# Kernel optimization log

Hardware: AMD Instinct MI355X
Metric: run time of the kernel (lower is better)

## Reference

```python
import jax, jax.numpy as jnp
import numpy as np

N = 200000   # active voxels
K = 27       # 3^3 kernel offsets
C = 64       # feature channels (in == out -> residual is Identity)
EPS = 1e-5   # BatchNorm eps (torch default)


def setup_inputs() -> dict:
    key = jax.random.key(0)
    k0, k1, k2, k3 = jax.random.split(key, 4)
    x = jax.random.normal(k0, (N, C), dtype=jnp.float32)
    # neighbor map: for each output voxel and kernel offset, index of input voxel
    nbr_idx = jax.random.randint(k1, (N, K), 0, N, dtype=jnp.int64)
    W1 = jax.random.normal(k2, (K, C, C), dtype=jnp.float32) * 0.05
    W2 = jax.random.normal(k3, (K, C, C), dtype=jnp.float32) * 0.05
    gamma1 = jnp.ones((C,), jnp.float32)
    beta1 = jnp.zeros((C,), jnp.float32)
    gamma2 = jnp.ones((C,), jnp.float32)
    beta2 = jnp.zeros((C,), jnp.float32)
    return {"x": x, "nbr_idx": nbr_idx, "W1": W1, "gamma1": gamma1,
            "beta1": beta1, "W2": W2, "gamma2": gamma2, "beta2": beta2}


def batchnorm(x, gamma, beta):
    # train-mode BatchNorm1d over the voxel axis (biased variance)
    mu = x.mean(axis=0)
    var = x.var(axis=0)
    return (x - mu) * jax.lax.rsqrt(var + EPS) * gamma + beta


def sparse_conv(x, nbr_idx, W):
    # gather-GEMM-scatter sparse conv, streamed over the 27 kernel offsets
    # x: [N, Cin], nbr_idx: [N, K], W: [K, Cin, Cout]
    def body(acc, kw):
        idx, Wk = kw                      # idx: [N], Wk: [Cin, Cout]
        return acc + x[idx] @ Wk, None
    acc0 = jnp.zeros((x.shape[0], W.shape[2]), x.dtype)
    acc, _ = jax.lax.scan(body, acc0, (nbr_idx.T, W))
    return acc


def reference(x, nbr_idx, W1, gamma1, beta1, W2, gamma2, beta2):
    residual = x  # in_features == out_features -> Identity residual
    out = sparse_conv(jax.nn.relu(batchnorm(x, gamma1, beta1)), nbr_idx, W1)
    out = sparse_conv(jax.nn.relu(batchnorm(out, gamma2, beta2)), nbr_idx, W2)
    return out + residual
```

## Files before the change

kernel.cpp:

```cpp
#include <hip/hip_runtime.h>


#define KOFF 27

typedef __bf16 bf16x8 __attribute__((ext_vector_type(8)));
typedef float floatx4 __attribute__((ext_vector_type(4)));

__device__ __forceinline__ unsigned short f2bf(float x) {
    union { float f; unsigned int u; } v; v.f = x;
    unsigned int u = v.u;
    unsigned int r = u + 0x7FFFu + ((u >> 16) & 1u);
    return (unsigned short)(r >> 16);
}
__device__ __forceinline__ float bf2f(unsigned short s) {
    union { float f; unsigned int u; } v; v.u = ((unsigned int)s) << 16; return v.f;
}

__global__ void prep2(const float* __restrict__ W1, const float* __restrict__ W2,
                      unsigned short* __restrict__ W1f, unsigned short* __restrict__ W2f,
                      const float* __restrict__ x, float* __restrict__ stats,
                      int total) {
    int b = blockIdx.x, t = threadIdx.x;
    if (b < 54) {
        __shared__ float sW[64 * 68];
        int k = b % 27;
        const float* src = (b < 27 ? W1 : W2) + k * 4096;
        unsigned short* dst = (b < 27 ? W1f : W2f) + (size_t)k * 4096;
        #pragma unroll
        for (int i = 0; i < 4; ++i) {
            int i4 = t + i * 256;
            float4 v = ((const float4*)src)[i4];
            int f = i4 * 4, r = f >> 6, c = f & 63;
            sW[r * 68 + c]     = v.x;
            sW[r * 68 + c + 1] = v.y;
            sW[r * 68 + c + 2] = v.z;
            sW[r * 68 + c + 3] = v.w;
        }
        __syncthreads();
        int fi = (t >> 5) & 7, ct = fi >> 1, ks = fi & 1;
        unsigned short o[16];
        #pragma unroll
        for (int d = 0; d < 2; ++d) {
            int lane2 = (t * 2 + d) & 63, q = lane2 >> 4, l15 = lane2 & 15;
            #pragma unroll
            for (int j = 0; j < 8; ++j) {
                int cin = ks * 32 + q * 8 + j, cout = ct * 16 + l15;
                o[d * 8 + j] = f2bf(sW[cin * 68 + cout]);
            }
        }
        ((uint4*)(dst + t * 16))[0] = *(const uint4*)(o);
        ((uint4*)(dst + t * 16))[1] = *(const uint4*)(o + 8);
        return;
    }
    __shared__ float s[128];
    if (t < 128) s[t] = 0.f;
    __syncthreads();
    int i = (b - 54) * 256 + t;
    int stride = (gridDim.x - 54) * 256;
    int c = i & 63;
    float s1 = 0.f, s2 = 0.f;
    for (; i < total; i += stride) { float v = x[i]; s1 += v; s2 += v * v; }
    atomicAdd(&s[c], s1);
    atomicAdd(&s[64 + c], s2);
    __syncthreads();
    if (t < 64) { atomicAdd(&stats[t], s[t]); atomicAdd(&stats[64 + t], s[64 + t]); }
}

__global__ void bn_relu_f32(const float* __restrict__ in, const float* __restrict__ sums,
                            const float* __restrict__ gamma, const float* __restrict__ beta,
                            unsigned short* __restrict__ out, int total4, float invN) {
    __shared__ float sab[128];
    int t = threadIdx.x;
    if (t < 64) {
        float mu  = sums[t] * invN;
        float var = fmaxf(sums[64 + t] * invN - mu * mu, 0.f);
        float a   = gamma[t] * rsqrtf(var + 1e-5f);
        sab[t] = a; sab[64 + t] = beta[t] - mu * a;
    }
    __syncthreads();
    int i = blockIdx.x * blockDim.x + t;
    int stride = gridDim.x * blockDim.x;
    for (; i < total4; i += stride) {
        float4 v = ((const float4*)in)[i];
        int c0 = (i << 2) & 63;
        ushort4 o;
        o.x = f2bf(fmaxf(sab[c0]     * v.x + sab[64 + c0],     0.f));
        o.y = f2bf(fmaxf(sab[c0 + 1] * v.y + sab[64 + c0 + 1], 0.f));
        o.z = f2bf(fmaxf(sab[c0 + 2] * v.z + sab[64 + c0 + 2], 0.f));
        o.w = f2bf(fmaxf(sab[c0 + 3] * v.w + sab[64 + c0 + 3], 0.f));
        ((ushort4*)out)[i] = o;
    }
}

__global__ void bn_relu_b16(const unsigned short* __restrict__ in, const float* __restrict__ sums,
                            const float* __restrict__ gamma, const float* __restrict__ beta,
                            unsigned short* __restrict__ out, int total8, float invN) {
    __shared__ float sab[128];
    int t = threadIdx.x;
    if (t < 64) {
        float mu  = sums[t] * invN;
        float var = fmaxf(sums[64 + t] * invN - mu * mu, 0.f);
        float a   = gamma[t] * rsqrtf(var + 1e-5f);
        sab[t] = a; sab[64 + t] = beta[t] - mu * a;
    }
    __syncthreads();
    int i = blockIdx.x * blockDim.x + t;
    int stride = gridDim.x * blockDim.x;
    for (; i < total8; i += stride) {
        uint4 v = ((const uint4*)in)[i];
        int c0 = (i << 3) & 63;
        unsigned int w[4] = {v.x, v.y, v.z, v.w};
        unsigned int o[4];
        #pragma unroll
        for (int p = 0; p < 4; ++p) {
            float f0 = bf2f((unsigned short)(w[p] & 0xffff));
            float f1 = bf2f((unsigned short)(w[p] >> 16));
            int c = c0 + p * 2;
            unsigned short r0 = f2bf(fmaxf(sab[c]     * f0 + sab[64 + c],     0.f));
            unsigned short r1 = f2bf(fmaxf(sab[c + 1] * f1 + sab[64 + c + 1], 0.f));
            o[p] = (unsigned int)r0 | ((unsigned int)r1 << 16);
        }
        ((uint4*)out)[i] = make_uint4(o[0], o[1], o[2], o[3]);
    }
}

#define MFMA(a, b, c) __builtin_amdgcn_mfma_f32_16x16x32_bf16(a, b, c, 0, 0, 0)
#define WAIT_LGKM0() __builtin_amdgcn_s_waitcnt(0xC07F)

__global__ __launch_bounds__(256, 4) void spconv(
        const unsigned short* __restrict__ h,
        const int* __restrict__ idx,
        const unsigned short* __restrict__ Wf,
        unsigned short* __restrict__ outb,
        float* __restrict__ outf,
        const float* __restrict__ resid,
        float* __restrict__ stats,
        int N) {
    __shared__ unsigned short sB[2][4096];
    __shared__ float sE[128 * 68];
    __shared__ float sred[128];
    int t = threadIdx.x, lane = t & 63, wid = t >> 6;
    int q = lane >> 4, l15 = lane & 15;
    int base = blockIdx.x * 128;
    if (t < 128) sred[t] = 0.f;

    int r0 = base + wid * 32 + l15;
    int r1 = r0 + 16;
    const int* ip0 = idx + (size_t)min(r0, N - 1) * KOFF;
    const int* ip1 = idx + (size_t)min(r1, N - 1) * KOFF;
    int qo = q * 8;

    floatx4 acc[2][4];
    #pragma unroll
    for (int a_ = 0; a_ < 2; ++a_)
        #pragma unroll
        for (int b_ = 0; b_ < 4; ++b_)
            acc[a_][b_] = floatx4{0.f, 0.f, 0.f, 0.f};

    bf16x8 A0[4], A1[4], A2[4];
    {
        int g0 = ip0[0], g1 = ip1[0];
        const unsigned short* p0 = h + ((size_t)g0 << 6) + qo;
        const unsigned short* p1 = h + ((size_t)g1 << 6) + qo;
        A0[0] = *(const bf16x8*)p0; A0[1] = *(const bf16x8*)(p0 + 32);
        A0[2] = *(const bf16x8*)p1; A0[3] = *(const bf16x8*)(p1 + 32);
        g0 = ip0[1]; g1 = ip1[1];
        p0 = h + ((size_t)g0 << 6) + qo;
        p1 = h + ((size_t)g1 << 6) + qo;
        A1[0] = *(const bf16x8*)p0; A1[1] = *(const bf16x8*)(p0 + 32);
        A1[2] = *(const bf16x8*)p1; A1[3] = *(const bf16x8*)(p1 + 32);
    }
    int gc0 = ip0[2], gc1 = ip1[2];

    const uint4* Wf4 = (const uint4*)Wf;
    int bo = wid * 128 + lane * 2;
    uint4 bs0 = Wf4[bo], bs1 = Wf4[bo + 1];
    ((uint4*)sB[0])[bo] = bs0; ((uint4*)sB[0])[bo + 1] = bs1;
    bs0 = Wf4[512 + bo]; bs1 = Wf4[512 + bo + 1];

#define COMPUTE(ACUR, CB) {                                                    \
    const bf16x8* bp = (const bf16x8*)sB[CB];                                  \
    bf16x8 f0 = bp[lane], f1 = bp[64 + lane], f2 = bp[128 + lane], f3 = bp[192 + lane]; \
    acc[0][0] = MFMA(ACUR[0], f0, acc[0][0]); acc[0][0] = MFMA(ACUR[1], f1, acc[0][0]); \
    acc[0][1] = MFMA(ACUR[0], f2, acc[0][1]); acc[0][1] = MFMA(ACUR[1], f3, acc[0][1]); \
    acc[1][0] = MFMA(ACUR[2], f0, acc[1][0]); acc[1][0] = MFMA(ACUR[3], f1, acc[1][0]); \
    acc[1][1] = MFMA(ACUR[2], f2, acc[1][1]); acc[1][1] = MFMA(ACUR[3], f3, acc[1][1]); \
    f0 = bp[256 + lane]; f1 = bp[320 + lane]; f2 = bp[384 + lane]; f3 = bp[448 + lane]; \
    acc[0][2] = MFMA(ACUR[0], f0, acc[0][2]); acc[0][2] = MFMA(ACUR[1], f1, acc[0][2]); \
    acc[0][3] = MFMA(ACUR[0], f2, acc[0][3]); acc[0][3] = MFMA(ACUR[1], f3, acc[0][3]); \
    acc[1][2] = MFMA(ACUR[2], f0, acc[1][2]); acc[1][2] = MFMA(ACUR[3], f1, acc[1][2]); \
    acc[1][3] = MFMA(ACUR[2], f2, acc[1][3]); acc[1][3] = MFMA(ACUR[3], f3, acc[1][3]); \
}

#define BODY_FULL(ACUR, ALD, KRT, CB, NB) {                                    \
    WAIT_LGKM0();                                                              \
    __builtin_amdgcn_s_barrier();                                              \
    ((uint4*)sB[NB])[bo] = bs0; ((uint4*)sB[NB])[bo + 1] = bs1;                \
    bs0 = Wf4[((KRT) + 2) * 512 + bo]; bs1 = Wf4[((KRT) + 2) * 512 + bo + 1];  \
    {                                                                          \
        const unsigned short* p0 = h + ((size_t)gc0 << 6) + qo;                \
        const unsigned short* p1 = h + ((size_t)gc1 << 6) + qo;                \
        ALD[0] = *(const bf16x8*)p0; ALD[1] = *(const bf16x8*)(p0 + 32);       \
        ALD[2] = *(const bf16x8*)p1; ALD[3] = *(const bf16x8*)(p1 + 32);       \
    }                                                                          \
    gc0 = ip0[(KRT) + 3]; gc1 = ip1[(KRT) + 3];                                \
    COMPUTE(ACUR, CB)                                                          \
}

    #pragma unroll 1
    for (int kk = 0; kk < 24; kk += 6) {
        BODY_FULL(A0, A2, kk + 0, 0, 1)
        BODY_FULL(A1, A0, kk + 1, 1, 0)
        BODY_FULL(A2, A1, kk + 2, 0, 1)
        BODY_FULL(A0, A2, kk + 3, 1, 0)
        BODY_FULL(A1, A0, kk + 4, 0, 1)
        BODY_FULL(A2, A1, kk + 5, 1, 0)
    }
    {
        WAIT_LGKM0();
        __builtin_amdgcn_s_barrier();
        ((uint4*)sB[1])[bo] = bs0; ((uint4*)sB[1])[bo + 1] = bs1;
        bs0 = Wf4[26 * 512 + bo]; bs1 = Wf4[26 * 512 + bo + 1];
        {
            const unsigned short* p0 = h + ((size_t)gc0 << 6) + qo;
            const unsigned short* p1 = h + ((size_t)gc1 << 6) + qo;
            A2[0] = *(const bf16x8*)p0; A2[1] = *(const bf16x8*)(p0 + 32);
            A2[2] = *(const bf16x8*)p1; A2[3] = *(const bf16x8*)(p1 + 32);
        }
        COMPUTE(A0, 0)
    }
    {
        WAIT_LGKM0();
        __builtin_amdgcn_s_barrier();
        ((uint4*)sB[0])[bo] = bs0; ((uint4*)sB[0])[bo + 1] = bs1;
        COMPUTE(A1, 1)
    }
    {
        WAIT_LGKM0();
        __builtin_amdgcn_s_barrier();
        COMPUTE(A2, 0)
    }
#undef BODY_FULL
#undef COMPUTE

    if (stats) {
        #pragma unroll
        for (int ct = 0; ct < 4; ++ct) {
            float s1 = 0.f, s2 = 0.f;
            #pragma unroll
            for (int rt = 0; rt < 2; ++rt)
                #pragma unroll
                for (int r = 0; r < 4; ++r) {
                    int rowc = base + wid * 32 + rt * 16 + q * 4 + r;
                    float vv = (rowc < N) ? acc[rt][ct][r] : 0.f;
                    s1 += vv; s2 += vv * vv;
                }
            s1 += __shfl_xor(s1, 16); s2 += __shfl_xor(s2, 16);
            s1 += __shfl_xor(s1, 32); s2 += __shfl_xor(s2, 32);
            if (q == 0) {
                atomicAdd(&sred[ct * 16 + l15], s1);
                atomicAdd(&sred[64 + ct * 16 + l15], s2);
            }
        }
    }

    #pragma unroll
    for (int rt = 0; rt < 2; ++rt)
        #pragma unroll
        for (int ct = 0; ct < 4; ++ct)
            #pragma unroll
            for (int r = 0; r < 4; ++r)
                sE[(wid * 32 + rt * 16 + q * 4 + r) * 68 + ct * 16 + l15] = acc[rt][ct][r];
    __syncthreads();
    if (stats && t < 64) {
        atomicAdd(&stats[t], sred[t]);
        atomicAdd(&stats[64 + t], sred[64 + t]);
    }

    int row = t >> 1, half = t & 1;
    int grow = base + row;
    if (grow < N) {
        const float* sp = sE + row * 68 + half * 32;
        if (outb) {
            unsigned short o[32];
            #pragma unroll
            for (int j = 0; j < 32; ++j) o[j] = f2bf(sp[j]);
            unsigned short* op = outb + ((size_t)grow << 6) + half * 32;
            ((uint4*)op)[0] = *(const uint4*)(o);
            ((uint4*)op)[1] = *(const uint4*)(o + 8);
            ((uint4*)op)[2] = *(const uint4*)(o + 16);
            ((uint4*)op)[3] = *(const uint4*)(o + 24);
        } else {
            const float* rp = resid + ((size_t)grow << 6) + half * 32;
            float* op = outf + ((size_t)grow << 6) + half * 32;
            #pragma unroll
            for (int j = 0; j < 8; ++j) {
                float4 v = *(const float4*)(sp + j * 4);
                float4 rv = *(const float4*)(rp + j * 4);
                v.x += rv.x; v.y += rv.y; v.z += rv.z; v.w += rv.w;
                *(float4*)(op + j * 4) = v;
            }
        }
    }
}

extern "C" void kernel_launch(void* const* d_in, const int* in_sizes, int n_in,
                              void* d_out, int out_size, void* d_ws, size_t ws_size,
                              hipStream_t stream) {
    const float* x      = (const float*)d_in[0];
    const int*   nbr    = (const int*)  d_in[1];
    const float* W1     = (const float*)d_in[2];
    const float* gamma1 = (const float*)d_in[3];
    const float* beta1  = (const float*)d_in[4];
    const float* W2     = (const float*)d_in[5];
    const float* gamma2 = (const float*)d_in[6];
    const float* beta2  = (const float*)d_in[7];
    float* out = (float*)d_out;

    int N = in_sizes[0] / 64;
    float invN = 1.0f / (float)N;

    char* ws = (char*)d_ws;
    float*          stats = (float*)ws;
    unsigned short* W1f   = (unsigned short*)(ws + 4096);
    unsigned short* W2f   = W1f + 110592;
    unsigned short* hbuf  = W2f + 110592;
    unsigned short* out1b = hbuf + (size_t)N * 64;

    int nb = (N + 127) / 128;

    hipMemsetAsync(stats, 0, 2048, stream);
    prep2<<<54 + 512, 256, 0, stream>>>(W1, W2, W1f, W2f, x, stats, N * 64);
    bn_relu_f32<<<768, 256, 0, stream>>>(x, stats, gamma1, beta1, hbuf, N * 16, invN);
    spconv<<<nb, 256, 0, stream>>>(hbuf, nbr, W1f, out1b, nullptr, nullptr, stats + 256, N);
    bn_relu_b16<<<768, 256, 0, stream>>>(out1b, stats + 256, gamma2, beta2, hbuf, N * 8, invN);
    spconv<<<nb, 256, 0, stream>>>(hbuf, nbr, W2f, nullptr, out, x, nullptr, N);
}
```

Before: 425.3 us.

## Alias weight buffer and epilogue staging in one LDS arena, epilogue in halves

Shared memory drops from separate double-buffered weight tiles plus a 128x68 float staging tile to one arena of about 17KB. The staging tile now holds 64 rows and the epilogue writes out in two passes of half the block each. Weight tile loads are re-indexed to coalesced 16-byte stripes. The goal is to cut LDS per block so more blocks fit per CU and hide gather latency, at the cost of extra barriers in the epilogue.

New measurement: 422.9 us. About the same (-0.5%).

```diff
diff --git a/kernel.cpp b/kernel.cpp
--- a/kernel.cpp
+++ b/kernel.cpp
@@ -136,9 +136,11 @@
         const float* __restrict__ resid,
         float* __restrict__ stats,
         int N) {
-    __shared__ unsigned short sB[2][4096];
-    __shared__ float sE[128 * 68];
+    __shared__ float4 arena[1088];
     __shared__ float sred[128];
+    unsigned short* sBb = (unsigned short*)arena;
+    float* sE = (float*)arena;
+
     int t = threadIdx.x, lane = t & 63, wid = t >> 6;
     int q = lane >> 4, l15 = lane & 15;
     int base = blockIdx.x * 128;
@@ -173,13 +175,13 @@
     int gc0 = ip0[2], gc1 = ip1[2];
 
     const uint4* Wf4 = (const uint4*)Wf;
-    int bo = wid * 128 + lane * 2;
-    uint4 bs0 = Wf4[bo], bs1 = Wf4[bo + 1];
-    ((uint4*)sB[0])[bo] = bs0; ((uint4*)sB[0])[bo + 1] = bs1;
-    bs0 = Wf4[512 + bo]; bs1 = Wf4[512 + bo + 1];
+    int so = wid * 64 + lane;
+    uint4 bs0 = Wf4[so], bs1 = Wf4[256 + so];
+    ((uint4*)sBb)[so] = bs0; ((uint4*)sBb)[256 + so] = bs1;
+    bs0 = Wf4[512 + so]; bs1 = Wf4[512 + 256 + so];
 
 #define COMPUTE(ACUR, CB) {                                                    \
-    const bf16x8* bp = (const bf16x8*)sB[CB];                                  \
+    const bf16x8* bp = (const bf16x8*)(sBb + (CB) * 4096);                     \
     bf16x8 f0 = bp[lane], f1 = bp[64 + lane], f2 = bp[128 + lane], f3 = bp[192 + lane]; \
     acc[0][0] = MFMA(ACUR[0], f0, acc[0][0]); acc[0][0] = MFMA(ACUR[1], f1, acc[0][0]); \
     acc[0][1] = MFMA(ACUR[0], f2, acc[0][1]); acc[0][1] = MFMA(ACUR[1], f3, acc[0][1]); \
@@ -195,8 +197,9 @@
 #define BODY_FULL(ACUR, ALD, KRT, CB, NB) {                                    \
     WAIT_LGKM0();                                                              \
     __builtin_amdgcn_s_barrier();                                              \
-    ((uint4*)sB[NB])[bo] = bs0; ((uint4*)sB[NB])[bo + 1] = bs1;                \
-    bs0 = Wf4[((KRT) + 2) * 512 + bo]; bs1 = Wf4[((KRT) + 2) * 512 + bo + 1];  \
+    ((uint4*)sBb)[(NB) * 512 + so] = bs0;                                      \
+    ((uint4*)sBb)[(NB) * 512 + 256 + so] = bs1;                                \
+    bs0 = Wf4[((KRT) + 2) * 512 + so]; bs1 = Wf4[((KRT) + 2) * 512 + 256 + so];\
     {                                                                          \
         const unsigned short* p0 = h + ((size_t)gc0 << 6) + qo;                \
         const unsigned short* p1 = h + ((size_t)gc1 << 6) + qo;                \
@@ -219,8 +222,8 @@
     {
         WAIT_LGKM0();
         __builtin_amdgcn_s_barrier();
-        ((uint4*)sB[1])[bo] = bs0; ((uint4*)sB[1])[bo + 1] = bs1;
-        bs0 = Wf4[26 * 512 + bo]; bs1 = Wf4[26 * 512 + bo + 1];
+        ((uint4*)sBb)[512 + so] = bs0; ((uint4*)sBb)[512 + 256 + so] = bs1;
+        bs0 = Wf4[26 * 512 + so]; bs1 = Wf4[26 * 512 + 256 + so];
         {
             const unsigned short* p0 = h + ((size_t)gc0 << 6) + qo;
             const unsigned short* p1 = h + ((size_t)gc1 << 6) + qo;
@@ -232,7 +235,7 @@
     {
         WAIT_LGKM0();
         __builtin_amdgcn_s_barrier();
-        ((uint4*)sB[0])[bo] = bs0; ((uint4*)sB[0])[bo + 1] = bs1;
+        ((uint4*)sBb)[so] = bs0; ((uint4*)sBb)[256 + so] = bs1;
         COMPUTE(A1, 1)
     }
     {
@@ -264,43 +267,49 @@
         }
     }
 
+    __syncthreads();
+
     #pragma unroll
-    for (int rt = 0; rt < 2; ++rt)
-        #pragma unroll
-        for (int ct = 0; ct < 4; ++ct)
+    for (int hf = 0; hf < 2; ++hf) {
+        if ((wid >> 1) == hf) {
+            int lrow0 = (wid & 1) * 32;
             #pragma unroll
-            for (int r = 0; r < 4; ++r)
-                sE[(wid * 32 + rt * 16 + q * 4 + r) * 68 + ct * 16 + l15] = acc[rt][ct][r];
-    __syncthreads();
-    if (stats && t < 64) {
-        atomicAdd(&stats[t], sred[t]);
-        atomicAdd(&stats[64 + t], sred[64 + t]);
-    }
-
-    int row = t >> 1, half = t & 1;
-    int grow = base + row;
-    if (grow < N) {
-        const float* sp = sE + row * 68 + half * 32;
-        if (outb) {
-            unsigned short o[32];
-            #pragma unroll
-            for (int j = 0; j < 32; ++j) o[j] = f2bf(sp[j]);
-            unsigned short* op = outb + ((size_t)grow << 6) + half * 32;
-            ((uint4*)op)[0] = *(const uint4*)(o);
-            ((uint4*)op)[1] = *(const uint4*)(o + 8);
-            ((uint4*)op)[2] = *(const uint4*)(o + 16);
-            ((uint4*)op)[3] = *(const uint4*)(o + 24);
-        } else {
-            const float* rp = resid + ((size_t)grow << 6) + half * 32;
-            float* op = outf + ((size_t)grow << 6) + half * 32;
-            #pragma unroll
-            for (int j = 0; j < 8; ++j) {
-                float4 v = *(const float4*)(sp + j * 4);
-                float4 rv = *(const float4*)(rp + j * 4);
-                v.x += rv.x; v.y += rv.y; v.z += rv.z; v.w += rv.w;
-                *(float4*)(op + j * 4) = v;
+            for (int rt = 0; rt < 2; ++rt)
+                #pragma unroll
+                for (int ct = 0; ct < 4; ++ct)
+                    #pragma unroll
+                    for (int r = 0; r < 4; ++r)
+                        sE[(lrow0 + rt * 16 + q * 4 + r) * 68 + ct * 16 + l15] = acc[rt][ct][r];
+        }
+        __syncthreads();
+        if (hf == 0 && stats && t < 64) {
+            atomicAdd(&stats[t], sred[t]);
+            atomicAdd(&stats[64 + t], sred[64 + t]);
+        }
+        int rr = t >> 2, cc = t & 3;
+        int grow = base + hf * 64 + rr;
+        if (grow < N) {
+            const float* sp = sE + rr * 68 + cc * 16;
+            if (outb) {
+                unsigned short o[16];
+                #pragma unroll
+                for (int j = 0; j < 16; ++j) o[j] = f2bf(sp[j]);
+                unsigned short* op = outb + ((size_t)grow << 6) + cc * 16;
+                ((uint4*)op)[0] = *(const uint4*)(o);
+                ((uint4*)op)[1] = *(const uint4*)(o + 8);
+            } else {
+                const float* rp = resid + ((size_t)grow << 6) + cc * 16;
+                float* op = outf + ((size_t)grow << 6) + cc * 16;
+                #pragma unroll
+                for (int j = 0; j < 4; ++j) {
+                    float4 v = *(const float4*)(sp + j * 4);
+                    float4 rv = *(const float4*)(rp + j * 4);
+                    v.x += rv.x; v.y += rv.y; v.z += rv.z; v.w += rv.w;
+                    *(float4*)(op + j * 4) = v;
+                }
             }
         }
+        if (hf == 0) __syncthreads();
     }
 }
 
```
